# Kernel tuning notes

Hardware: AMD Instinct MI355X
Metric: run time of the kernel (lower is better)

Reference implementation:

```python
import jax, jax.numpy as jnp
import numpy as np

H = 64; W = 64; P = 16; NPH = 4; NPW = 4; PH = 16; PW = 16; ZD = 32; HD = 1024; UD = 3; B = 256


def affine_grid(theta, Ho, Wo):
    # torch F.affine_grid, align_corners=False. theta [N,2,3] -> grid [N,Ho,Wo,2]
    xs = (2.0 * jnp.arange(Wo, dtype=theta.dtype) + 1.0) / Wo - 1.0
    ys = (2.0 * jnp.arange(Ho, dtype=theta.dtype) + 1.0) / Ho - 1.0
    X, Y = jnp.meshgrid(xs, ys)  # [Ho,Wo] each, x varies along last axis
    base = jnp.stack([X, Y, jnp.ones_like(X)], axis=-1)  # [Ho,Wo,3]
    return jnp.einsum('nij,hwj->nhwi', theta, base)


def grid_sample(img, grid):
    # torch F.grid_sample bilinear, padding_mode='zeros', align_corners=False
    # img [N,H,W], grid [N,Ho,Wo,2] in [-1,1]
    Hi, Wi = img.shape[1], img.shape[2]
    x = (grid[..., 0] + 1.0) * Wi / 2.0 - 0.5
    y = (grid[..., 1] + 1.0) * Hi / 2.0 - 0.5
    x0 = jnp.floor(x); y0 = jnp.floor(y)
    wx = x - x0; wy = y - y0

    def gather(ix, iy):
        valid = (ix >= 0) & (ix < Wi) & (iy >= 0) & (iy < Hi)
        ixc = jnp.clip(ix, 0, Wi - 1).astype(jnp.int32)
        iyc = jnp.clip(iy, 0, Hi - 1).astype(jnp.int32)
        v = jax.vmap(lambda im, yy, xx: im[yy, xx])(img, iyc, ixc)
        return jnp.where(valid, v, 0.0)

    return (gather(x0, y0) * (1 - wx) * (1 - wy)
            + gather(x0 + 1, y0) * wx * (1 - wy)
            + gather(x0, y0 + 1) * (1 - wx) * wy
            + gather(x0 + 1, y0 + 1) * wx * wy)


def rot_tr(u):
    # rotTrMatrix: u [N,3] (angle, tx, ty) -> [N,2,3]
    c = jnp.cos(u[:, 0]); s = jnp.sin(u[:, 0])
    R = jnp.stack([jnp.stack([c, -s], -1), jnp.stack([s, c], -1)], -2)  # [N,2,2]
    return jnp.concatenate([R, u[:, 1:3, None]], axis=2)


def anchor_theta():
    # anchor_move: identity rotation + per-part grid-cell-center translations
    tx = (np.arange(NPW) * (W / NPW) + W / NPW / 2) / W - 0.5
    ty = (np.arange(NPH) * (H / NPH) + H / NPH / 2) / H - 0.5
    th = np.tile(np.concatenate([np.eye(2), np.zeros((2, 1))], axis=1)[None], (P, 1, 1)).astype(np.float32)
    for k in range(P):
        th[k, 0, 2] = tx[k % NPW]
        th[k, 1, 2] = ty[k // NPW]
    return jnp.asarray(th)


def forward(inputs, W1, b1, W2, b2, Wum, bum, Wuv, buv, Wgm, bgm, Wgv, bgv, Wz, M, eps_u, eps_g):
    hid = jax.nn.relu(inputs.reshape(-1, H * W) @ W1 + b1)
    hid = jax.nn.relu(hid @ W2 + b2)
    # global transform distribution (note: F.threshold(x,-6,6) -> 6 where x<=-6)
    gmu = jnp.tanh(hid @ Wgm + bgm)
    gpre = hid @ Wgv + bgv
    gvar = jnp.exp(jnp.where(gpre > -6.0, gpre, 6.0))
    gu = gmu + gvar * eps_g  # sample_u uses mu + var*eps (var, not std) as in source
    # per-part transform distribution (F.threshold(x,-6,-6) -> clamp below at -6)
    umu = jnp.tanh(hid @ Wum + bum)
    upre = hid @ Wuv + buv
    uvar = jnp.exp(jnp.where(upre > -6.0, upre, -6.0))
    u = (umu + uvar * eps_u).reshape(-1, UD)  # [B*P,3]
    # decode parts (input is ones, as in source)
    parts = jax.nn.sigmoid(jnp.ones((B, ZD), inputs.dtype) @ Wz).reshape(B * P, PH, PW)
    padh = (H - PH) // 2; padw = (W - PW) // 2
    parts = jnp.pad(parts, ((0, 0), (padh, H - PH - padh), (padw, W - PW - padw)))
    # anchor placement of parts and kernel masks
    th_a = jnp.tile(anchor_theta(), (B, 1, 1))  # [B*P,2,3], part-minor ordering
    g_a = affine_grid(th_a, H, W)
    parts = grid_sample(parts, g_a)                     # [B*P,H,W]
    KM = grid_sample(M[:B * P].reshape(B * P, H, W), g_a)
    # per-part rotation+translation for parts; translation-only for kernel
    theta = rot_tr(u)                                   # [B*P,2,3]
    g = affine_grid(theta, H, W)
    eye = jnp.broadcast_to(jnp.eye(2, dtype=theta.dtype), (B * P, 2, 2))
    theta_K = jnp.concatenate([eye, theta[:, :, 2:3]], axis=2)
    g_K = affine_grid(theta_K, H, W)
    KM = grid_sample(KM, g_K).reshape(B, P, H, W)
    xp = grid_sample(parts, g).reshape(B, P, H, W)
    # masked weighted compositing
    num = jnp.sum(xp * KM, axis=1)
    den = jnp.sum(KM, axis=1)
    den = jnp.where(den == 0.0, 1.0, den)
    x = num / den
    # global transform
    theta_g = rot_tr(gu)
    g_g = affine_grid(theta_g, H, W)
    return grid_sample(x, g_g)[:, None]  # [B,1,H,W]


def setup_inputs() -> dict:
    key = jax.random.key(0)
    ks = jax.random.split(key, 18)

    def lin(k, fin, fout):
        return jax.random.normal(k, (fin, fout), jnp.float32) / np.sqrt(fin)

    return {
        'inputs': jax.random.uniform(ks[0], (B, H * W), jnp.float32),
        'W1': lin(ks[1], H * W, HD), 'b1': jnp.zeros((HD,), jnp.float32),
        'W2': lin(ks[2], HD, HD), 'b2': jnp.zeros((HD,), jnp.float32),
        'Wum': lin(ks[3], HD, P * UD), 'bum': jnp.zeros((P * UD,), jnp.float32),
        'Wuv': lin(ks[4], HD, P * UD), 'buv': jnp.zeros((P * UD,), jnp.float32),
        'Wgm': lin(ks[5], HD, UD), 'bgm': jnp.zeros((UD,), jnp.float32),
        'Wgv': lin(ks[6], HD, UD), 'bgv': jnp.zeros((UD,), jnp.float32),
        'Wz': lin(ks[7], ZD, P * PH * PW),
        'M': jax.random.uniform(ks[8], (B * P, 1, H, W), jnp.float32),
        'eps_u': jax.random.normal(ks[9], (B, P * UD), jnp.float32),
        'eps_g': jax.random.normal(ks[10], (B, UD), jnp.float32),
    }


def reference(inputs, W1, b1, W2, b2, Wum, bum, Wuv, buv, Wgm, bgm, Wgv, bgv, Wz, M, eps_u, eps_g):
    return forward(inputs, W1, b1, W2, b2, Wum, bum, Wuv, buv, Wgm, bgm, Wgv, bgv, Wz, M, eps_u, eps_g)
```

## Files before the change

### kernel.cpp

```cpp
#include <hip/hip_runtime.h>
#include <math.h>

#define SPLITK 8

typedef __bf16 bf16x8 __attribute__((ext_vector_type(8)));
typedef float  f32x4  __attribute__((ext_vector_type(4)));
typedef float  f32x16 __attribute__((ext_vector_type(16)));

__device__ inline unsigned short bf16rne(float x) {
    unsigned int u = __float_as_uint(x);
    unsigned int r = u + 0x7FFFu + ((u >> 16) & 1u);
    return (unsigned short)(r >> 16);
}
__device__ inline float bf16tof(unsigned short h) {
    return __uint_as_float(((unsigned int)h) << 16);
}

__global__ __launch_bounds__(256) void prep_all(
    const float* __restrict__ inputs,
    const float* __restrict__ W1, const float* __restrict__ W2,
    const float* __restrict__ Wum, const float* __restrict__ Wuv,
    const float* __restrict__ Wgm, const float* __restrict__ Wgv,
    const float* __restrict__ Wz,
    unsigned short* __restrict__ Ahi, unsigned short* __restrict__ Alo,
    unsigned short* __restrict__ W1Thi, unsigned short* __restrict__ W1Tlo,
    unsigned short* __restrict__ W2Thi, unsigned short* __restrict__ W2Tlo,
    float* __restrict__ WT, float* __restrict__ partsb)
{
    __shared__ float t[32][33];
    int bid = blockIdx.x;
    int tid = threadIdx.x;
    if (bid < 4096 || (bid >= 5120 && bid < 6144)) {
        const float* W = (bid < 4096) ? W1 : W2;
        unsigned short* Thi = (bid < 4096) ? W1Thi : W2Thi;
        unsigned short* Tlo = (bid < 4096) ? W1Tlo : W2Tlo;
        int K = (bid < 4096) ? 4096 : 1024;
        int b2 = (bid < 4096) ? bid : (bid - 5120);
        int n0 = (b2 & 31) * 32, k0 = (b2 >> 5) * 32;
        int c = tid & 31, r0 = tid >> 5;
#pragma unroll
        for (int i = 0; i < 4; i++)
            t[r0 + 8 * i][c] = W[(size_t)(k0 + r0 + 8 * i) * 1024 + n0 + c];
        __syncthreads();
        int kk = tid & 31, n1 = tid >> 5;
#pragma unroll
        for (int i = 0; i < 4; i++) {
            float x = t[kk][n1 + 8 * i];
            unsigned short h = bf16rne(x);
            unsigned short l = bf16rne(x - bf16tof(h));
            size_t o = (size_t)(n0 + n1 + 8 * i) * K + k0 + kk;
            Thi[o] = h;
            Tlo[o] = l;
        }
    } else if (bid < 5120) {
        int id = ((bid - 4096) * 256 + tid) * 4;
        float4 x = *(const float4*)(inputs + id);
        ushort4 h, l;
        h.x = bf16rne(x.x); l.x = bf16rne(x.x - bf16tof(h.x));
        h.y = bf16rne(x.y); l.y = bf16rne(x.y - bf16tof(h.y));
        h.z = bf16rne(x.z); l.z = bf16rne(x.z - bf16tof(h.z));
        h.w = bf16rne(x.w); l.w = bf16rne(x.w - bf16tof(h.w));
        *(ushort4*)(Ahi + id) = h;
        *(ushort4*)(Alo + id) = l;
    } else if (bid < 6552) {
        int id = (bid - 6144) * 256 + tid;
        int o = id >> 10;
        int k = id & 1023;
        float v;
        if (o < 48)       v = Wum[k * 48 + o];
        else if (o < 96)  v = Wuv[k * 48 + (o - 48)];
        else if (o < 99)  v = Wgm[k * 3 + (o - 96)];
        else              v = Wgv[k * 3 + (o - 99)];
        WT[id] = v;
    } else {
        int idx = (bid - 6552) * 256 + tid;
        float s = 0.f;
#pragma unroll
        for (int z = 0; z < 32; z++) s += Wz[z * 4096 + idx];
        partsb[idx] = 1.f / (1.f + expf(-s));
    }
}

__global__ __launch_bounds__(256) void gemm_bf16x3(
    const unsigned short* __restrict__ Ahi, const unsigned short* __restrict__ Alo,
    const unsigned short* __restrict__ Bhi, const unsigned short* __restrict__ Blo,
    float* __restrict__ psum, int K, int kchunk)
{
    __shared__ unsigned short Ah[4096], Al[4096], Bh[4096], Bl[4096];
    int tid = threadIdx.x;
    int n0 = blockIdx.x * 64, m0 = blockIdx.y * 64;
    int kb = blockIdx.z * kchunk;
    int wid = tid >> 6, lane = tid & 63;
    int wm = wid & 1, wn = wid >> 1;
    int lr = lane & 31, hi = lane >> 5;

    int r0 = tid >> 3, ch0 = tid & 7;
    int r1 = (tid + 256) >> 3, ch1 = (tid + 256) & 7;
    int l0 = r0 * 64 + 8 * (ch0 ^ (r0 & 7));
    int l1 = r1 * 64 + 8 * (ch1 ^ (r1 & 7));
    size_t ga0 = (size_t)(m0 + r0) * K + kb + ch0 * 8;
    size_t ga1 = (size_t)(m0 + r1) * K + kb + ch1 * 8;
    size_t gb0 = (size_t)(n0 + r0) * K + kb + ch0 * 8;
    size_t gb1 = (size_t)(n0 + r1) * K + kb + ch1 * 8;

    f32x16 acc_hh = {}, acc_hl = {}, acc_lh = {};

    int nkt = kchunk >> 6;
    uint4 vah0, vah1, val0, val1, vbh0, vbh1, vbl0, vbl1;
    vah0 = *(const uint4*)(Ahi + ga0);
    vah1 = *(const uint4*)(Ahi + ga1);
    val0 = *(const uint4*)(Alo + ga0);
    val1 = *(const uint4*)(Alo + ga1);
    vbh0 = *(const uint4*)(Bhi + gb0);
    vbh1 = *(const uint4*)(Bhi + gb1);
    vbl0 = *(const uint4*)(Blo + gb0);
    vbl1 = *(const uint4*)(Blo + gb1);

    int basea = (wm * 32 + lr) * 64;
    int baseb = (wn * 32 + lr) * 64;
    int sw = lr & 7;

    for (int kt = 0; kt < nkt; kt++) {
        __syncthreads();
        *(uint4*)(Ah + l0) = vah0;
        *(uint4*)(Ah + l1) = vah1;
        *(uint4*)(Al + l0) = val0;
        *(uint4*)(Al + l1) = val1;
        *(uint4*)(Bh + l0) = vbh0;
        *(uint4*)(Bh + l1) = vbh1;
        *(uint4*)(Bl + l0) = vbl0;
        *(uint4*)(Bl + l1) = vbl1;
        __syncthreads();
        if (kt + 1 < nkt) {
            size_t o = (size_t)(kt + 1) * 64;
            vah0 = *(const uint4*)(Ahi + ga0 + o);
            vah1 = *(const uint4*)(Ahi + ga1 + o);
            val0 = *(const uint4*)(Alo + ga0 + o);
            val1 = *(const uint4*)(Alo + ga1 + o);
            vbh0 = *(const uint4*)(Bhi + gb0 + o);
            vbh1 = *(const uint4*)(Bhi + gb1 + o);
            vbl0 = *(const uint4*)(Blo + gb0 + o);
            vbl1 = *(const uint4*)(Blo + gb1 + o);
        }
#pragma unroll
        for (int s = 0; s < 4; s++) {
            int cidx = 8 * (((s << 1) + hi) ^ sw);
            bf16x8 afh = *(const bf16x8*)(Ah + basea + cidx);
            bf16x8 afl = *(const bf16x8*)(Al + basea + cidx);
            bf16x8 bfh = *(const bf16x8*)(Bh + baseb + cidx);
            bf16x8 bfl = *(const bf16x8*)(Bl + baseb + cidx);
            acc_hh = __builtin_amdgcn_mfma_f32_32x32x16_bf16(afh, bfh, acc_hh, 0, 0, 0);
            acc_hl = __builtin_amdgcn_mfma_f32_32x32x16_bf16(afh, bfl, acc_hl, 0, 0, 0);
            acc_lh = __builtin_amdgcn_mfma_f32_32x32x16_bf16(afl, bfh, acc_lh, 0, 0, 0);
        }
    }

    float* op = psum + (size_t)blockIdx.z * (256 * 1024);
    int colg = n0 + wn * 32 + lr;
#pragma unroll
    for (int r = 0; r < 16; r++) {
        int rowl = (r & 3) + 8 * (r >> 2) + 4 * hi;
        float v = acc_hh[r] + acc_hl[r] + acc_lh[r];
        op[(size_t)(m0 + wm * 32 + rowl) * 1024 + colg] = v;
    }
}

__global__ __launch_bounds__(256) void reduce_bias_relu_split(
    const float* __restrict__ psum, const float* __restrict__ bias,
    unsigned short* __restrict__ hi, unsigned short* __restrict__ lo)
{
    int i = (blockIdx.x * 256 + threadIdx.x) * 4;
    float4 v = *(const float4*)(psum + i);
#pragma unroll
    for (int s = 1; s < SPLITK; s++) {
        float4 t = *(const float4*)(psum + (size_t)s * 262144 + i);
        v.x += t.x; v.y += t.y; v.z += t.z; v.w += t.w;
    }
    float4 bb = *(const float4*)(bias + (i & 1023));
    v.x = fmaxf(v.x + bb.x, 0.f);
    v.y = fmaxf(v.y + bb.y, 0.f);
    v.z = fmaxf(v.z + bb.z, 0.f);
    v.w = fmaxf(v.w + bb.w, 0.f);
    ushort4 h, l;
    h.x = bf16rne(v.x); l.x = bf16rne(v.x - bf16tof(h.x));
    h.y = bf16rne(v.y); l.y = bf16rne(v.y - bf16tof(h.y));
    h.z = bf16rne(v.z); l.z = bf16rne(v.z - bf16tof(h.z));
    h.w = bf16rne(v.w); l.w = bf16rne(v.w - bf16tof(h.w));
    *(ushort4*)(hi + i) = h;
    *(ushort4*)(lo + i) = l;
}

__global__ __launch_bounds__(512) void heads_v3(
    const float* __restrict__ psum, const float* __restrict__ b2,
    const float* __restrict__ WT,
    const float* __restrict__ bum, const float* __restrict__ buv,
    const float* __restrict__ bgm, const float* __restrict__ bgv,
    const float* __restrict__ eps_u, const float* __restrict__ eps_g,
    float* __restrict__ u_out, float* __restrict__ gu_out)
{
    int b = blockIdx.x;
    int tid = threadIdx.x;
    int w = tid >> 6, l = tid & 63;

    float4 hr[4];
#pragma unroll
    for (int i = 0; i < 4; i++) {
        int k = b * 1024 + i * 256 + l * 4;
        float4 acc = *(const float4*)(psum + k);
#pragma unroll
        for (int s = 1; s < SPLITK; s++) {
            float4 t = *(const float4*)(psum + (size_t)s * 262144 + k);
            acc.x += t.x; acc.y += t.y; acc.z += t.z; acc.w += t.w;
        }
        float4 bb = *(const float4*)(b2 + i * 256 + l * 4);
        acc.x = fmaxf(acc.x + bb.x, 0.f);
        acc.y = fmaxf(acc.y + bb.y, 0.f);
        acc.z = fmaxf(acc.z + bb.z, 0.f);
        acc.w = fmaxf(acc.w + bb.w, 0.f);
        hr[i] = acc;
    }

    int o = w;
    int rm = (o < 48) ? o : (48 + o);
    int rv = (o < 48) ? (o + 48) : (51 + o);
    float4 wm[4], wv[4];
    {
        const float* wp = WT + rm * 1024 + l * 4;
#pragma unroll
        for (int i = 0; i < 4; i++) wm[i] = *(const float4*)(wp + i * 256);
        wp = WT + rv * 1024 + l * 4;
#pragma unroll
        for (int i = 0; i < 4; i++) wv[i] = *(const float4*)(wp + i * 256);
    }

    while (o < 51) {
        int onext = o + 8;
        float4 wmn[4], wvn[4];
        if (onext < 51) {
            int rm2 = (onext < 48) ? onext : (48 + onext);
            int rv2 = (onext < 48) ? (onext + 48) : (51 + onext);
            const float* wp = WT + rm2 * 1024 + l * 4;
#pragma unroll
            for (int i = 0; i < 4; i++) wmn[i] = *(const float4*)(wp + i * 256);
            wp = WT + rv2 * 1024 + l * 4;
#pragma unroll
            for (int i = 0; i < 4; i++) wvn[i] = *(const float4*)(wp + i * 256);
        }
        float am = 0.f, av = 0.f;
#pragma unroll
        for (int i = 0; i < 4; i++) {
            am = fmaf(hr[i].x, wm[i].x, am);
            am = fmaf(hr[i].y, wm[i].y, am);
            am = fmaf(hr[i].z, wm[i].z, am);
            am = fmaf(hr[i].w, wm[i].w, am);
            av = fmaf(hr[i].x, wv[i].x, av);
            av = fmaf(hr[i].y, wv[i].y, av);
            av = fmaf(hr[i].z, wv[i].z, av);
            av = fmaf(hr[i].w, wv[i].w, av);
        }
#pragma unroll
        for (int s = 32; s; s >>= 1) {
            am += __shfl_xor(am, s, 64);
            av += __shfl_xor(av, s, 64);
        }
        if (l == 0) {
            if (o < 48) {
                float umu = tanhf(am + bum[o]);
                float uvar = expf(fmaxf(av + buv[o], -6.f));
                u_out[b * 48 + o] = umu + uvar * eps_u[b * 48 + o];
            } else {
                int n = o - 48;
                float gmu = tanhf(am + bgm[n]);
                float gpre = av + bgv[n];
                float gvar = expf(gpre > -6.f ? gpre : 6.f);
                gu_out[b * 3 + n] = gmu + gvar * eps_g[b * 3 + n];
            }
        }
#pragma unroll
        for (int i = 0; i < 4; i++) { wm[i] = wmn[i]; wv[i] = wvn[i]; }
        o = onext;
    }
}

__global__ __launch_bounds__(1024) void composite_final(
    const float* __restrict__ M, const float* __restrict__ parts,
    const float* __restrict__ u, const float* __restrict__ gu,
    float* __restrict__ out)
{
    __shared__ float patch[4096];
    __shared__ float plane[2][4096];
    __shared__ float pc[16], psn[16], ptx[16], pty[16], pwx[16], pwy[16];
    __shared__ int pix[16], piy[16];
    int b = blockIdx.x;
    int tid = threadIdx.x;

    for (int i = tid; i < 4096; i += 1024) patch[i] = parts[i];
    if (tid < 16) {
        const float* up = u + (b * 16 + tid) * 3;
        float ang = up[0];
        pc[tid] = cosf(ang);
        psn[tid] = sinf(ang);
        float tx = up[1], ty = up[2];
        ptx[tid] = tx;
        pty[tid] = ty;
        float ax = fminf(fmaxf(32.f * tx, -16384.f), 16384.f);
        float fax = floorf(ax);
        pwx[tid] = ax - fax;
        pix[tid] = (int)fax;
        float ay = fminf(fmaxf(32.f * ty, -16384.f), 16384.f);
        float fay = floorf(ay);
        pwy[tid] = ay - fay;
        piy[tid] = (int)fay;
    }

    const float* Mb = M + ((size_t)(b * 16) << 12);
    ((float4*)plane[0])[tid] = ((const float4*)Mb)[tid];
    float4 pfn = ((const float4*)(Mb + 4096))[tid];
    __syncthreads();

    int j = tid & 63;
    int i0 = (tid >> 6) * 4;
    float xnv = (float)(2 * j + 1) * (1.f / 64.f) - 1.f;
    float ynv0 = (float)(2 * i0 + 1) * (1.f / 64.f) - 1.f;

    float num[4] = {}, den[4] = {};

    for (int p = 0; p < 16; p++) {
        int cur = p & 1;
        if (p + 1 < 16) ((float4*)plane[1 - cur])[tid] = pfn;
        if (p + 2 < 16) pfn = ((const float4*)(Mb + ((size_t)(p + 2) << 12)))[tid];

        int dx = 8 * (p & 3) - 12;
        int dy = 8 * (p >> 2) - 12;
        float c = pc[p], s = psn[p], tx = ptx[p], ty = pty[p];
        float wx = pwx[p], wy = pwy[p];
        int ix = pix[p], iy = piy[p];
        int iY = iy + dy;

        int x0 = j + ix;
        int X = x0 + dx;
        bool vc0 = ((unsigned)x0 < 64u) && ((unsigned)X < 64u);
        bool vc1 = ((unsigned)(x0 + 1) < 64u) && ((unsigned)(X + 1) < 64u);
        float w0 = vc0 ? (1.f - wx) : 0.f;
        float w1 = vc1 ? wx : 0.f;
        int Xc0 = min(max(X, 0), 63);
        int Xc1 = min(max(X + 1, 0), 63);

        const float* pl = plane[cur];
        float R[5];
#pragma unroll
        for (int r = 0; r < 5; r++) {
            int i = i0 + r;
            int ri = i + iY;
            bool vr = ((unsigned)(i + iy) < 64u) && ((unsigned)ri < 64u);
            int ric = min(max(ri, 0), 63);
            const float* row = pl + (ric << 6);
            float val = fmaf(w0, row[Xc0], w1 * row[Xc1]);
            R[r] = vr ? val : 0.f;
        }

        float gx0 = fmaf(-s, ynv0, fmaf(c, xnv, tx));
        float gy0 = fmaf(c, ynv0, fmaf(s, xnv, ty));
        float xs = fmaf(gx0, 32.f, 31.5f);
        float ysv = fmaf(gy0, 32.f, 31.5f);
        int ox = 24 - dx, oy = 24 - dy;
        float oxf = (float)ox, oyf = (float)oy;
        const float* pp = patch + (p << 8);
#pragma unroll
        for (int r = 0; r < 4; r++) {
            float km = fmaf(wy, R[r + 1] - R[r], R[r]);
            den[r] += km;

            if (xs >= oxf - 1.f && xs < oxf + 16.f &&
                ysv >= oyf - 1.f && ysv < oyf + 16.f) {
                float xf = floorf(xs), yf = floorf(ysv);
                float wxx = xs - xf, wyy = ysv - yf;
                int a0 = (int)yf - oy;
                int b0c = (int)xf - ox;
                float v00 = 0.f, v10 = 0.f, v01 = 0.f, v11 = 0.f;
                if ((unsigned)a0 < 16u) {
                    const float* pr = pp + a0 * 16;
                    if ((unsigned)b0c < 16u) v00 = pr[b0c];
                    if ((unsigned)(b0c + 1) < 16u) v10 = pr[b0c + 1];
                }
                if ((unsigned)(a0 + 1) < 16u) {
                    const float* pr = pp + (a0 + 1) * 16;
                    if ((unsigned)b0c < 16u) v01 = pr[b0c];
                    if ((unsigned)(b0c + 1) < 16u) v11 = pr[b0c + 1];
                }
                float top = fmaf(wxx, v10 - v00, v00);
                float bot = fmaf(wxx, v11 - v01, v01);
                float xp = fmaf(wyy, bot - top, top);
                num[r] = fmaf(xp, km, num[r]);
            }
            xs -= s;
            ysv += c;
        }
        __syncthreads();
    }

    float* xl = plane[0];
#pragma unroll
    for (int r = 0; r < 4; r++) {
        float d = (den[r] == 0.f) ? 1.f : den[r];
        xl[(i0 + r) * 64 + j] = num[r] / d;
    }
    __syncthreads();

    float ang = gu[b * 3 + 0], gtx = gu[b * 3 + 1], gty = gu[b * 3 + 2];
    float cg = cosf(ang), sg = sinf(ang);
    float* ob = out + ((size_t)b << 12);
#pragma unroll
    for (int r = 0; r < 4; r++) {
        int i = i0 + r;
        float ynv = (float)(2 * i + 1) * (1.f / 64.f) - 1.f;
        float gx = cg * xnv - sg * ynv + gtx;
        float gy = sg * xnv + cg * ynv + gty;
        gx = fminf(fmaxf(gx, -8.f), 8.f);
        gy = fminf(fmaxf(gy, -8.f), 8.f);
        float xs = fmaf(gx, 32.f, 31.5f);
        float ysv = fmaf(gy, 32.f, 31.5f);
        float xf = floorf(xs), yf = floorf(ysv);
        float wx = xs - xf, wy = ysv - yf;
        int x0 = (int)xf, y0 = (int)yf;
        float v00 = 0.f, v10 = 0.f, v01 = 0.f, v11 = 0.f;
        bool vx0 = (unsigned)x0 < 64u, vx1 = (unsigned)(x0 + 1) < 64u;
        if ((unsigned)y0 < 64u) {
            const float* row = xl + y0 * 64;
            if (vx0) v00 = row[x0];
            if (vx1) v10 = row[x0 + 1];
        }
        if ((unsigned)(y0 + 1) < 64u) {
            const float* row = xl + (y0 + 1) * 64;
            if (vx0) v01 = row[x0];
            if (vx1) v11 = row[x0 + 1];
        }
        float top = fmaf(wx, v10 - v00, v00);
        float bot = fmaf(wx, v11 - v01, v01);
        ob[i * 64 + j] = fmaf(wy, bot - top, top);
    }
}

extern "C" void kernel_launch(void* const* d_in, const int* in_sizes, int n_in,
                              void* d_out, int out_size, void* d_ws, size_t ws_size,
                              hipStream_t stream)
{
    (void)in_sizes; (void)n_in; (void)out_size; (void)ws_size;
    const float* inputs = (const float*)d_in[0];
    const float* W1  = (const float*)d_in[1];
    const float* b1  = (const float*)d_in[2];
    const float* W2  = (const float*)d_in[3];
    const float* b2  = (const float*)d_in[4];
    const float* Wum = (const float*)d_in[5];
    const float* bum = (const float*)d_in[6];
    const float* Wuv = (const float*)d_in[7];
    const float* buv = (const float*)d_in[8];
    const float* Wgm = (const float*)d_in[9];
    const float* bgm = (const float*)d_in[10];
    const float* Wgv = (const float*)d_in[11];
    const float* bgv = (const float*)d_in[12];
    const float* Wz  = (const float*)d_in[13];
    const float* Mm  = (const float*)d_in[14];
    const float* eps_u = (const float*)d_in[15];
    const float* eps_g = (const float*)d_in[16];

    float* ws = (float*)d_ws;
    float* psum      = ws;
    float* u_buf     = ws + 2097152;
    float* gu_buf    = u_buf + 12288;
    float* parts_buf = gu_buf + 768;
    float* WTh_buf   = parts_buf + 4096;
    unsigned short* us = (unsigned short*)(WTh_buf + 104448);
    unsigned short* Ahi   = us;
    unsigned short* Alo   = Ahi + 1048576;
    unsigned short* W1Thi = Alo + 1048576;
    unsigned short* W1Tlo = W1Thi + 4194304;
    unsigned short* W2Thi = W1Tlo + 4194304;
    unsigned short* W2Tlo = W2Thi + 1048576;
    unsigned short* H1hi  = W2Tlo + 1048576;
    unsigned short* H1lo  = H1hi + 262144;

    prep_all<<<6568, 256, 0, stream>>>(inputs, W1, W2, Wum, Wuv, Wgm, Wgv, Wz,
                                       Ahi, Alo, W1Thi, W1Tlo, W2Thi, W2Tlo,
                                       WTh_buf, parts_buf);

    gemm_bf16x3<<<dim3(16, 4, SPLITK), 256, 0, stream>>>(Ahi, Alo, W1Thi, W1Tlo,
                                                         psum, 4096, 4096 / SPLITK);
    reduce_bias_relu_split<<<256, 256, 0, stream>>>(psum, b1, H1hi, H1lo);
    gemm_bf16x3<<<dim3(16, 4, SPLITK), 256, 0, stream>>>(H1hi, H1lo, W2Thi, W2Tlo,
                                                         psum, 1024, 1024 / SPLITK);
    heads_v3<<<256, 512, 0, stream>>>(psum, b2, WTh_buf, bum, buv, bgm, bgv,
                                      eps_u, eps_g, u_buf, gu_buf);
    composite_final<<<256, 1024, 0, stream>>>(Mm, parts_buf, u_buf, gu_buf,
                                              (float*)d_out);
}
```

Measured before the change: 198.0 us.

## Fuse all stages into one persistent kernel with software grid barriers

Replaces the six separate launches (prep, two split-K GEMMs, reduce, heads, composite) with a single persistent 256-block, 1024-thread kernel that separates phases with an atomic grid barrier. The goal is to remove launch gaps and to keep the head outputs in shared memory instead of going through global buffers. The GEMM tiles drop to a 32-wide K step, and only two of the four thread groups in each block do GEMM work, which halves the active compute during the GEMM phases. It also depends on all 256 blocks being co-resident, or the spin barrier can deadlock.

Measured after the change: 342.8 us. +73.1%, slower.

```diff
diff --git a/kernel.cpp b/kernel.cpp
--- a/kernel.cpp
+++ b/kernel.cpp
@@ -1,306 +1,323 @@
 #include <hip/hip_runtime.h>
 #include <math.h>
 
+#define NBLK 256
 #define SPLITK 8
+#define PSUM_STRIDE 262144
 
 typedef __bf16 bf16x8 __attribute__((ext_vector_type(8)));
-typedef float  f32x4  __attribute__((ext_vector_type(4)));
 typedef float  f32x16 __attribute__((ext_vector_type(16)));
 
-__device__ inline unsigned short bf16rne(float x) {
+__device__ __forceinline__ unsigned short bf16rne(float x) {
     unsigned int u = __float_as_uint(x);
     unsigned int r = u + 0x7FFFu + ((u >> 16) & 1u);
     return (unsigned short)(r >> 16);
 }
-__device__ inline float bf16tof(unsigned short h) {
+__device__ __forceinline__ float bf16tof(unsigned short h) {
     return __uint_as_float(((unsigned int)h) << 16);
 }
 
-__global__ __launch_bounds__(256) void prep_all(
-    const float* __restrict__ inputs,
-    const float* __restrict__ W1, const float* __restrict__ W2,
-    const float* __restrict__ Wum, const float* __restrict__ Wuv,
-    const float* __restrict__ Wgm, const float* __restrict__ Wgv,
-    const float* __restrict__ Wz,
+__device__ __forceinline__ void grid_barrier(unsigned int* bar) {
+    __syncthreads();
+    if (threadIdx.x == 0) {
+        __threadfence();
+        unsigned int gen = __hip_atomic_load(bar + 32, __ATOMIC_RELAXED, __HIP_MEMORY_SCOPE_AGENT);
+        unsigned int arrived = __hip_atomic_fetch_add(bar, 1u, __ATOMIC_ACQ_REL, __HIP_MEMORY_SCOPE_AGENT);
+        if (arrived == (unsigned int)(NBLK - 1)) {
+            __hip_atomic_store(bar, 0u, __ATOMIC_RELAXED, __HIP_MEMORY_SCOPE_AGENT);
+            __hip_atomic_store(bar + 32, gen + 1u, __ATOMIC_RELEASE, __HIP_MEMORY_SCOPE_AGENT);
+        } else {
+            long cap = 0;
+            while (__hip_atomic_load(bar + 32, __ATOMIC_ACQUIRE, __HIP_MEMORY_SCOPE_AGENT) == gen) {
+                __builtin_amdgcn_s_sleep(2);
+                if (++cap > 200000000L) break;
+            }
+        }
+        __threadfence();
+    }
+    __syncthreads();
+}
+
+__device__ __forceinline__ void gemm_job(
+    const unsigned short* __restrict__ Ahi, const unsigned short* __restrict__ Alo,
+    const unsigned short* __restrict__ Bhi, const unsigned short* __restrict__ Blo,
+    float* __restrict__ psum, int K, int kchunk, int job, int t,
+    unsigned short* lds, bool active)
+{
+    unsigned short* Ah = lds;
+    unsigned short* Al = lds + 2048;
+    unsigned short* Bh = lds + 4096;
+    unsigned short* Bl = lds + 6144;
+    int z = job & 7, xy = job >> 3;
+    int n0 = (xy & 15) * 64, m0 = (xy >> 4) * 64;
+    int kb = z * kchunk;
+    int wid = t >> 6, lane = t & 63;
+    int wm = wid & 1, wn = wid >> 1;
+    int lr = lane & 31, hi = lane >> 5;
+
+    int r0 = t >> 2, ch0 = t & 3;
+    int l0 = r0 * 32 + 8 * (ch0 ^ ((r0 >> 1) & 3));
+    size_t ga = (size_t)(m0 + r0) * K + kb + ch0 * 8;
+    size_t gb = (size_t)(n0 + r0) * K + kb + ch0 * 8;
+
+    f32x16 acc_hh = {}, acc_hl = {}, acc_lh = {};
+    int nkt = kchunk >> 5;
+
+    uint4 vah, val, vbh, vbl;
+    if (active) {
+        vah = *(const uint4*)(Ahi + ga);
+        val = *(const uint4*)(Alo + ga);
+        vbh = *(const uint4*)(Bhi + gb);
+        vbl = *(const uint4*)(Blo + gb);
+    }
+
+    int basea = (wm * 32 + lr) * 32;
+    int baseb = (wn * 32 + lr) * 32;
+    int sw = (lr >> 1) & 3;
+
+    for (int kt = 0; kt < nkt; kt++) {
+        __syncthreads();
+        if (active) {
+            *(uint4*)(Ah + l0) = vah;
+            *(uint4*)(Al + l0) = val;
+            *(uint4*)(Bh + l0) = vbh;
+            *(uint4*)(Bl + l0) = vbl;
+        }
+        __syncthreads();
+        if (active) {
+            if (kt + 1 < nkt) {
+                size_t o = (size_t)(kt + 1) * 32;
+                vah = *(const uint4*)(Ahi + ga + o);
+                val = *(const uint4*)(Alo + ga + o);
+                vbh = *(const uint4*)(Bhi + gb + o);
+                vbl = *(const uint4*)(Blo + gb + o);
+            }
+#pragma unroll
+            for (int s = 0; s < 2; s++) {
+                int ca = 8 * (((s << 1) + hi) ^ sw);
+                bf16x8 afh = *(const bf16x8*)(Ah + basea + ca);
+                bf16x8 afl = *(const bf16x8*)(Al + basea + ca);
+                bf16x8 bfh = *(const bf16x8*)(Bh + baseb + ca);
+                bf16x8 bfl = *(const bf16x8*)(Bl + baseb + ca);
+                acc_hh = __builtin_amdgcn_mfma_f32_32x32x16_bf16(afh, bfh, acc_hh, 0, 0, 0);
+                acc_hl = __builtin_amdgcn_mfma_f32_32x32x16_bf16(afh, bfl, acc_hl, 0, 0, 0);
+                acc_lh = __builtin_amdgcn_mfma_f32_32x32x16_bf16(afl, bfh, acc_lh, 0, 0, 0);
+            }
+        }
+    }
+    if (active) {
+        float* op = psum + (size_t)z * PSUM_STRIDE;
+        int colg = n0 + wn * 32 + lr;
+#pragma unroll
+        for (int r = 0; r < 16; r++) {
+            int rowl = (r & 3) + 8 * (r >> 2) + 4 * hi;
+            op[(size_t)(m0 + wm * 32 + rowl) * 1024 + colg] = acc_hh[r] + acc_hl[r] + acc_lh[r];
+        }
+    }
+}
+
+__global__ __launch_bounds__(1024) void mega(
+    const float* __restrict__ inputs, const float* __restrict__ W1,
+    const float* __restrict__ b1, const float* __restrict__ W2,
+    const float* __restrict__ b2,
+    const float* __restrict__ Wum, const float* __restrict__ bum,
+    const float* __restrict__ Wuv, const float* __restrict__ buv,
+    const float* __restrict__ Wgm, const float* __restrict__ bgm,
+    const float* __restrict__ Wgv, const float* __restrict__ bgv,
+    const float* __restrict__ Wz, const float* __restrict__ Mm,
+    const float* __restrict__ eps_u, const float* __restrict__ eps_g,
+    float* __restrict__ out,
+    unsigned int* __restrict__ bar,
+    float* __restrict__ psum, float* __restrict__ parts_buf, float* __restrict__ WT,
     unsigned short* __restrict__ Ahi, unsigned short* __restrict__ Alo,
     unsigned short* __restrict__ W1Thi, unsigned short* __restrict__ W1Tlo,
     unsigned short* __restrict__ W2Thi, unsigned short* __restrict__ W2Tlo,
-    float* __restrict__ WT, float* __restrict__ partsb)
+    unsigned short* __restrict__ H1hi, unsigned short* __restrict__ H1lo)
 {
-    __shared__ float t[32][33];
-    int bid = blockIdx.x;
+    __shared__ __align__(16) unsigned char smem[65536];
+    int blk = blockIdx.x;
+    if (blk >= NBLK) return;
     int tid = threadIdx.x;
-    if (bid < 4096 || (bid >= 5120 && bid < 6144)) {
-        const float* W = (bid < 4096) ? W1 : W2;
-        unsigned short* Thi = (bid < 4096) ? W1Thi : W2Thi;
-        unsigned short* Tlo = (bid < 4096) ? W1Tlo : W2Tlo;
-        int K = (bid < 4096) ? 4096 : 1024;
-        int b2 = (bid < 4096) ? bid : (bid - 5120);
-        int n0 = (b2 & 31) * 32, k0 = (b2 >> 5) * 32;
-        int c = tid & 31, r0 = tid >> 5;
-#pragma unroll
-        for (int i = 0; i < 4; i++)
-            t[r0 + 8 * i][c] = W[(size_t)(k0 + r0 + 8 * i) * 1024 + n0 + c];
-        __syncthreads();
-        int kk = tid & 31, n1 = tid >> 5;
-#pragma unroll
-        for (int i = 0; i < 4; i++) {
-            float x = t[kk][n1 + 8 * i];
-            unsigned short h = bf16rne(x);
-            unsigned short l = bf16rne(x - bf16tof(h));
-            size_t o = (size_t)(n0 + n1 + 8 * i) * K + k0 + kk;
-            Thi[o] = h;
-            Tlo[o] = l;
-        }
-    } else if (bid < 5120) {
-        int id = ((bid - 4096) * 256 + tid) * 4;
-        float4 x = *(const float4*)(inputs + id);
-        ushort4 h, l;
-        h.x = bf16rne(x.x); l.x = bf16rne(x.x - bf16tof(h.x));
-        h.y = bf16rne(x.y); l.y = bf16rne(x.y - bf16tof(h.y));
-        h.z = bf16rne(x.z); l.z = bf16rne(x.z - bf16tof(h.z));
-        h.w = bf16rne(x.w); l.w = bf16rne(x.w - bf16tof(h.w));
-        *(ushort4*)(Ahi + id) = h;
-        *(ushort4*)(Alo + id) = l;
-    } else if (bid < 6552) {
-        int id = (bid - 6144) * 256 + tid;
-        int o = id >> 10;
-        int k = id & 1023;
-        float v;
-        if (o < 48)       v = Wum[k * 48 + o];
-        else if (o < 96)  v = Wuv[k * 48 + (o - 48)];
-        else if (o < 99)  v = Wgm[k * 3 + (o - 96)];
-        else              v = Wgv[k * 3 + (o - 99)];
-        WT[id] = v;
-    } else {
-        int idx = (bid - 6552) * 256 + tid;
-        float s = 0.f;
-#pragma unroll
-        for (int z = 0; z < 32; z++) s += Wz[z * 4096 + idx];
-        partsb[idx] = 1.f / (1.f + expf(-s));
-    }
-}
-
-__global__ __launch_bounds__(256) void gemm_bf16x3(
-    const unsigned short* __restrict__ Ahi, const unsigned short* __restrict__ Alo,
-    const unsigned short* __restrict__ Bhi, const unsigned short* __restrict__ Blo,
-    float* __restrict__ psum, int K, int kchunk)
-{
-    __shared__ unsigned short Ah[4096], Al[4096], Bh[4096], Bl[4096];
-    int tid = threadIdx.x;
-    int n0 = blockIdx.x * 64, m0 = blockIdx.y * 64;
-    int kb = blockIdx.z * kchunk;
-    int wid = tid >> 6, lane = tid & 63;
-    int wm = wid & 1, wn = wid >> 1;
-    int lr = lane & 31, hi = lane >> 5;
-
-    int r0 = tid >> 3, ch0 = tid & 7;
-    int r1 = (tid + 256) >> 3, ch1 = (tid + 256) & 7;
-    int l0 = r0 * 64 + 8 * (ch0 ^ (r0 & 7));
-    int l1 = r1 * 64 + 8 * (ch1 ^ (r1 & 7));
-    size_t ga0 = (size_t)(m0 + r0) * K + kb + ch0 * 8;
-    size_t ga1 = (size_t)(m0 + r1) * K + kb + ch1 * 8;
-    size_t gb0 = (size_t)(n0 + r0) * K + kb + ch0 * 8;
-    size_t gb1 = (size_t)(n0 + r1) * K + kb + ch1 * 8;
-
-    f32x16 acc_hh = {}, acc_hl = {}, acc_lh = {};
-
-    int nkt = kchunk >> 6;
-    uint4 vah0, vah1, val0, val1, vbh0, vbh1, vbl0, vbl1;
-    vah0 = *(const uint4*)(Ahi + ga0);
-    vah1 = *(const uint4*)(Ahi + ga1);
-    val0 = *(const uint4*)(Alo + ga0);
-    val1 = *(const uint4*)(Alo + ga1);
-    vbh0 = *(const uint4*)(Bhi + gb0);
-    vbh1 = *(const uint4*)(Bhi + gb1);
-    vbl0 = *(const uint4*)(Blo + gb0);
-    vbl1 = *(const uint4*)(Blo + gb1);
-
-    int basea = (wm * 32 + lr) * 64;
-    int baseb = (wn * 32 + lr) * 64;
-    int sw = lr & 7;
-
-    for (int kt = 0; kt < nkt; kt++) {
-        __syncthreads();
-        *(uint4*)(Ah + l0) = vah0;
-        *(uint4*)(Ah + l1) = vah1;
-        *(uint4*)(Al + l0) = val0;
-        *(uint4*)(Al + l1) = val1;
-        *(uint4*)(Bh + l0) = vbh0;
-        *(uint4*)(Bh + l1) = vbh1;
-        *(uint4*)(Bl + l0) = vbl0;
-        *(uint4*)(Bl + l1) = vbl1;
-        __syncthreads();
-        if (kt + 1 < nkt) {
-            size_t o = (size_t)(kt + 1) * 64;
-            vah0 = *(const uint4*)(Ahi + ga0 + o);
-            vah1 = *(const uint4*)(Ahi + ga1 + o);
-            val0 = *(const uint4*)(Alo + ga0 + o);
-            val1 = *(const uint4*)(Alo + ga1 + o);
-            vbh0 = *(const uint4*)(Bhi + gb0 + o);
-            vbh1 = *(const uint4*)(Bhi + gb1 + o);
-            vbl0 = *(const uint4*)(Blo + gb0 + o);
-            vbl1 = *(const uint4*)(Blo + gb1 + o);
-        }
-#pragma unroll
-        for (int s = 0; s < 4; s++) {
-            int cidx = 8 * (((s << 1) + hi) ^ sw);
-            bf16x8 afh = *(const bf16x8*)(Ah + basea + cidx);
-            bf16x8 afl = *(const bf16x8*)(Al + basea + cidx);
-            bf16x8 bfh = *(const bf16x8*)(Bh + baseb + cidx);
-            bf16x8 bfl = *(const bf16x8*)(Bl + baseb + cidx);
-            acc_hh = __builtin_amdgcn_mfma_f32_32x32x16_bf16(afh, bfh, acc_hh, 0, 0, 0);
-            acc_hl = __builtin_amdgcn_mfma_f32_32x32x16_bf16(afh, bfl, acc_hl, 0, 0, 0);
-            acc_lh = __builtin_amdgcn_mfma_f32_32x32x16_bf16(afl, bfh, acc_lh, 0, 0, 0);
-        }
-    }
-
-    float* op = psum + (size_t)blockIdx.z * (256 * 1024);
-    int colg = n0 + wn * 32 + lr;
-#pragma unroll
-    for (int r = 0; r < 16; r++) {
-        int rowl = (r & 3) + 8 * (r >> 2) + 4 * hi;
-        float v = acc_hh[r] + acc_hl[r] + acc_lh[r];
-        op[(size_t)(m0 + wm * 32 + rowl) * 1024 + colg] = v;
-    }
-}
-
-__global__ __launch_bounds__(256) void reduce_bias_relu_split(
-    const float* __restrict__ psum, const float* __restrict__ bias,
-    unsigned short* __restrict__ hi, unsigned short* __restrict__ lo)
-{
-    int i = (blockIdx.x * 256 + threadIdx.x) * 4;
-    float4 v = *(const float4*)(psum + i);
-#pragma unroll
-    for (int s = 1; s < SPLITK; s++) {
-        float4 t = *(const float4*)(psum + (size_t)s * 262144 + i);
-        v.x += t.x; v.y += t.y; v.z += t.z; v.w += t.w;
-    }
-    float4 bb = *(const float4*)(bias + (i & 1023));
-    v.x = fmaxf(v.x + bb.x, 0.f);
-    v.y = fmaxf(v.y + bb.y, 0.f);
-    v.z = fmaxf(v.z + bb.z, 0.f);
-    v.w = fmaxf(v.w + bb.w, 0.f);
-    ushort4 h, l;
-    h.x = bf16rne(v.x); l.x = bf16rne(v.x - bf16tof(h.x));
-    h.y = bf16rne(v.y); l.y = bf16rne(v.y - bf16tof(h.y));
-    h.z = bf16rne(v.z); l.z = bf16rne(v.z - bf16tof(h.z));
-    h.w = bf16rne(v.w); l.w = bf16rne(v.w - bf16tof(h.w));
-    *(ushort4*)(hi + i) = h;
-    *(ushort4*)(lo + i) = l;
-}
-
-__global__ __launch_bounds__(512) void heads_v3(
-    const float* __restrict__ psum, const float* __restrict__ b2,
-    const float* __restrict__ WT,
-    const float* __restrict__ bum, const float* __restrict__ buv,
-    const float* __restrict__ bgm, const float* __restrict__ bgv,
-    const float* __restrict__ eps_u, const float* __restrict__ eps_g,
-    float* __restrict__ u_out, float* __restrict__ gu_out)
-{
-    int b = blockIdx.x;
-    int tid = threadIdx.x;
-    int w = tid >> 6, l = tid & 63;
-
-    float4 hr[4];
-#pragma unroll
-    for (int i = 0; i < 4; i++) {
-        int k = b * 1024 + i * 256 + l * 4;
-        float4 acc = *(const float4*)(psum + k);
-#pragma unroll
-        for (int s = 1; s < SPLITK; s++) {
-            float4 t = *(const float4*)(psum + (size_t)s * 262144 + k);
-            acc.x += t.x; acc.y += t.y; acc.z += t.z; acc.w += t.w;
-        }
-        float4 bb = *(const float4*)(b2 + i * 256 + l * 4);
-        acc.x = fmaxf(acc.x + bb.x, 0.f);
-        acc.y = fmaxf(acc.y + bb.y, 0.f);
-        acc.z = fmaxf(acc.z + bb.z, 0.f);
-        acc.w = fmaxf(acc.w + bb.w, 0.f);
-        hr[i] = acc;
-    }
-
-    int o = w;
-    int rm = (o < 48) ? o : (48 + o);
-    int rv = (o < 48) ? (o + 48) : (51 + o);
-    float4 wm[4], wv[4];
+    int g = tid >> 8;
+    int t = tid & 255;
+    int gid = blk * 1024 + tid;
+
     {
-        const float* wp = WT + rm * 1024 + l * 4;
-#pragma unroll
-        for (int i = 0; i < 4; i++) wm[i] = *(const float4*)(wp + i * 256);
-        wp = WT + rv * 1024 + l * 4;
-#pragma unroll
-        for (int i = 0; i < 4; i++) wv[i] = *(const float4*)(wp + i * 256);
-    }
-
-    while (o < 51) {
-        int onext = o + 8;
-        float4 wmn[4], wvn[4];
-        if (onext < 51) {
-            int rm2 = (onext < 48) ? onext : (48 + onext);
-            int rv2 = (onext < 48) ? (onext + 48) : (51 + onext);
-            const float* wp = WT + rm2 * 1024 + l * 4;
-#pragma unroll
-            for (int i = 0; i < 4; i++) wmn[i] = *(const float4*)(wp + i * 256);
-            wp = WT + rv2 * 1024 + l * 4;
-#pragma unroll
-            for (int i = 0; i < 4; i++) wvn[i] = *(const float4*)(wp + i * 256);
-        }
-        float am = 0.f, av = 0.f;
-#pragma unroll
-        for (int i = 0; i < 4; i++) {
-            am = fmaf(hr[i].x, wm[i].x, am);
-            am = fmaf(hr[i].y, wm[i].y, am);
-            am = fmaf(hr[i].z, wm[i].z, am);
-            am = fmaf(hr[i].w, wm[i].w, am);
-            av = fmaf(hr[i].x, wv[i].x, av);
-            av = fmaf(hr[i].y, wv[i].y, av);
-            av = fmaf(hr[i].z, wv[i].z, av);
-            av = fmaf(hr[i].w, wv[i].w, av);
-        }
-#pragma unroll
-        for (int s = 32; s; s >>= 1) {
-            am += __shfl_xor(am, s, 64);
-            av += __shfl_xor(av, s, 64);
-        }
-        if (l == 0) {
-            if (o < 48) {
-                float umu = tanhf(am + bum[o]);
-                float uvar = expf(fmaxf(av + buv[o], -6.f));
-                u_out[b * 48 + o] = umu + uvar * eps_u[b * 48 + o];
-            } else {
-                int n = o - 48;
-                float gmu = tanhf(am + bgm[n]);
-                float gpre = av + bgv[n];
-                float gvar = expf(gpre > -6.f ? gpre : 6.f);
-                gu_out[b * 3 + n] = gmu + gvar * eps_g[b * 3 + n];
-            }
-        }
-#pragma unroll
-        for (int i = 0; i < 4; i++) { wm[i] = wmn[i]; wv[i] = wvn[i]; }
-        o = onext;
-    }
-}
-
-__global__ __launch_bounds__(1024) void composite_final(
-    const float* __restrict__ M, const float* __restrict__ parts,
-    const float* __restrict__ u, const float* __restrict__ gu,
-    float* __restrict__ out)
-{
-    __shared__ float patch[4096];
-    __shared__ float plane[2][4096];
-    __shared__ float pc[16], psn[16], ptx[16], pty[16], pwx[16], pwy[16];
-    __shared__ int pix[16], piy[16];
-    int b = blockIdx.x;
-    int tid = threadIdx.x;
-
-    for (int i = tid; i < 4096; i += 1024) patch[i] = parts[i];
+        float (*tile)[33] = (float(*)[33])(smem + g * 4352);
+        for (int pass = 0; pass < 4; pass++) {
+            int b2t = blk * 16 + pass * 4 + g;
+            int n0 = (b2t & 31) * 32, k0 = (b2t >> 5) * 32;
+            int c = t & 31, r0 = t >> 5;
+#pragma unroll
+            for (int i = 0; i < 4; i++)
+                tile[r0 + 8 * i][c] = W1[(size_t)(k0 + r0 + 8 * i) * 1024 + n0 + c];
+            __syncthreads();
+            int kk = t & 31, n1 = t >> 5;
+#pragma unroll
+            for (int i = 0; i < 4; i++) {
+                float x = tile[kk][n1 + 8 * i];
+                unsigned short h = bf16rne(x);
+                unsigned short l = bf16rne(x - bf16tof(h));
+                size_t o = (size_t)(n0 + n1 + 8 * i) * 4096 + k0 + kk;
+                W1Thi[o] = h;
+                W1Tlo[o] = l;
+            }
+            __syncthreads();
+        }
+        {
+            int b2t = blk * 4 + g;
+            int n0 = (b2t & 31) * 32, k0 = (b2t >> 5) * 32;
+            int c = t & 31, r0 = t >> 5;
+#pragma unroll
+            for (int i = 0; i < 4; i++)
+                tile[r0 + 8 * i][c] = W2[(size_t)(k0 + r0 + 8 * i) * 1024 + n0 + c];
+            __syncthreads();
+            int kk = t & 31, n1 = t >> 5;
+#pragma unroll
+            for (int i = 0; i < 4; i++) {
+                float x = tile[kk][n1 + 8 * i];
+                unsigned short h = bf16rne(x);
+                unsigned short l = bf16rne(x - bf16tof(h));
+                size_t o = (size_t)(n0 + n1 + 8 * i) * 1024 + k0 + kk;
+                W2Thi[o] = h;
+                W2Tlo[o] = l;
+            }
+        }
+        {
+            int id = gid * 4;
+            float4 x = *(const float4*)(inputs + id);
+            ushort4 h, l;
+            h.x = bf16rne(x.x); l.x = bf16rne(x.x - bf16tof(h.x));
+            h.y = bf16rne(x.y); l.y = bf16rne(x.y - bf16tof(h.y));
+            h.z = bf16rne(x.z); l.z = bf16rne(x.z - bf16tof(h.z));
+            h.w = bf16rne(x.w); l.w = bf16rne(x.w - bf16tof(h.w));
+            *(ushort4*)(Ahi + id) = h;
+            *(ushort4*)(Alo + id) = l;
+        }
+        if (gid < 104448) {
+            int o = gid >> 10;
+            int k = gid & 1023;
+            float v;
+            if (o < 48)       v = Wum[k * 48 + o];
+            else if (o < 96)  v = Wuv[k * 48 + (o - 48)];
+            else if (o < 99)  v = Wgm[k * 3 + (o - 96)];
+            else              v = Wgv[k * 3 + (o - 99)];
+            WT[gid] = v;
+        }
+        if (gid < 4096) {
+            float s = 0.f;
+#pragma unroll
+            for (int z = 0; z < 32; z++) s += Wz[z * 4096 + gid];
+            parts_buf[gid] = 1.f / (1.f + expf(-s));
+        }
+    }
+    grid_barrier(bar);
+
+    gemm_job(Ahi, Alo, W1Thi, W1Tlo, psum, 4096, 4096 / SPLITK,
+             blk * 2 + (g & 1), t, (unsigned short*)(smem + g * 16384), g < 2);
+    grid_barrier(bar);
+
+    {
+        float v = psum[gid];
+#pragma unroll
+        for (int s = 1; s < SPLITK; s++) v += psum[(size_t)s * PSUM_STRIDE + gid];
+        v = fmaxf(v + b1[tid], 0.f);
+        unsigned short h = bf16rne(v);
+        unsigned short l = bf16rne(v - bf16tof(h));
+        H1hi[gid] = h;
+        H1lo[gid] = l;
+    }
+    grid_barrier(bar);
+
+    gemm_job(H1hi, H1lo, W2Thi, W2Tlo, psum, 1024, 1024 / SPLITK,
+             blk * 2 + (g & 1), t, (unsigned short*)(smem + g * 16384), g < 2);
+    grid_barrier(bar);
+
+    float* patch  = (float*)smem;
+    float* plane0 = (float*)(smem + 16384);
+    float* plane1 = (float*)(smem + 32768);
+    float* h2     = (float*)(smem + 49152);
+    float* u_raw  = (float*)(smem + 53248);
+    float* pc  = (float*)(smem + 53504);
+    float* psn = pc + 16;
+    float* ptx = pc + 32;
+    float* pty = pc + 48;
+    float* pwx = pc + 64;
+    float* pwy = pc + 80;
+    int*   pix = (int*)(pc + 96);
+    int*   piy = pix + 16;
+    int b = blk;
+
+    {
+        float v = psum[(size_t)b * 1024 + tid];
+#pragma unroll
+        for (int s = 1; s < SPLITK; s++)
+            v += psum[(size_t)s * PSUM_STRIDE + (size_t)b * 1024 + tid];
+        h2[tid] = fmaxf(v + b2[tid], 0.f);
+    }
+    for (int i = tid; i < 4096; i += 1024) patch[i] = parts_buf[i];
+    __syncthreads();
+    {
+        int w = tid >> 6, l = tid & 63;
+        const float4* h4 = (const float4*)h2;
+        float4 hr0 = h4[l], hr1 = h4[64 + l], hr2 = h4[128 + l], hr3 = h4[192 + l];
+        for (int o = w; o < 51; o += 16) {
+            int rm = (o < 48) ? o : (48 + o);
+            int rv = (o < 48) ? (o + 48) : (51 + o);
+            const float* wpm = WT + rm * 1024 + l * 4;
+            const float* wpv = WT + rv * 1024 + l * 4;
+            float4 wm0 = *(const float4*)(wpm);
+            float4 wm1 = *(const float4*)(wpm + 256);
+            float4 wm2 = *(const float4*)(wpm + 512);
+            float4 wm3 = *(const float4*)(wpm + 768);
+            float4 wv0 = *(const float4*)(wpv);
+            float4 wv1 = *(const float4*)(wpv + 256);
+            float4 wv2 = *(const float4*)(wpv + 512);
+            float4 wv3 = *(const float4*)(wpv + 768);
+            float am = 0.f, av = 0.f;
+            am = fmaf(hr0.x, wm0.x, am); am = fmaf(hr0.y, wm0.y, am);
+            am = fmaf(hr0.z, wm0.z, am); am = fmaf(hr0.w, wm0.w, am);
+            av = fmaf(hr0.x, wv0.x, av); av = fmaf(hr0.y, wv0.y, av);
+            av = fmaf(hr0.z, wv0.z, av); av = fmaf(hr0.w, wv0.w, av);
+            am = fmaf(hr1.x, wm1.x, am); am = fmaf(hr1.y, wm1.y, am);
+            am = fmaf(hr1.z, wm1.z, am); am = fmaf(hr1.w, wm1.w, am);
+            av = fmaf(hr1.x, wv1.x, av); av = fmaf(hr1.y, wv1.y, av);
+            av = fmaf(hr1.z, wv1.z, av); av = fmaf(hr1.w, wv1.w, av);
+            am = fmaf(hr2.x, wm2.x, am); am = fmaf(hr2.y, wm2.y, am);
+            am = fmaf(hr2.z, wm2.z, am); am = fmaf(hr2.w, wm2.w, am);
+            av = fmaf(hr2.x, wv2.x, av); av = fmaf(hr2.y, wv2.y, av);
+            av = fmaf(hr2.z, wv2.z, av); av = fmaf(hr2.w, wv2.w, av);
+            am = fmaf(hr3.x, wm3.x, am); am = fmaf(hr3.y, wm3.y, am);
+            am = fmaf(hr3.z, wm3.z, am); am = fmaf(hr3.w, wm3.w, am);
+            av = fmaf(hr3.x, wv3.x, av); av = fmaf(hr3.y, wv3.y, av);
+            av = fmaf(hr3.z, wv3.z, av); av = fmaf(hr3.w, wv3.w, av);
+#pragma unroll
+            for (int s = 32; s; s >>= 1) {
+                am += __shfl_xor(am, s, 64);
+                av += __shfl_xor(av, s, 64);
+            }
+            if (l == 0) {
+                if (o < 48) {
+                    float umu = tanhf(am + bum[o]);
+                    float uvar = expf(fmaxf(av + buv[o], -6.f));
+                    u_raw[o] = umu + uvar * eps_u[b * 48 + o];
+                } else {
+                    int n = o - 48;
+                    float gmu = tanhf(am + bgm[n]);
+                    float gpre = av + bgv[n];
+                    float gvar = expf(gpre > -6.f ? gpre : 6.f);
+                    u_raw[o] = gmu + gvar * eps_g[b * 3 + n];
+                }
+            }
+        }
+    }
+    __syncthreads();
+
     if (tid < 16) {
-        const float* up = u + (b * 16 + tid) * 3;
-        float ang = up[0];
+        float ang = u_raw[tid * 3 + 0];
+        float tx = u_raw[tid * 3 + 1], ty = u_raw[tid * 3 + 2];
         pc[tid] = cosf(ang);
         psn[tid] = sinf(ang);
-        float tx = up[1], ty = up[2];
         ptx[tid] = tx;
         pty[tid] = ty;
         float ax = fminf(fmaxf(32.f * tx, -16384.f), 16384.f);
@@ -312,9 +329,8 @@
         pwy[tid] = ay - fay;
         piy[tid] = (int)fay;
     }
-
-    const float* Mb = M + ((size_t)(b * 16) << 12);
-    ((float4*)plane[0])[tid] = ((const float4*)Mb)[tid];
+    const float* Mb = Mm + ((size_t)(b * 16) << 12);
+    ((float4*)plane0)[tid] = ((const float4*)Mb)[tid];
     float4 pfn = ((const float4*)(Mb + 4096))[tid];
     __syncthreads();
 
@@ -324,10 +340,11 @@
     float ynv0 = (float)(2 * i0 + 1) * (1.f / 64.f) - 1.f;
 
     float num[4] = {}, den[4] = {};
+    float* pl_cur = plane0;
+    float* pl_nxt = plane1;
 
     for (int p = 0; p < 16; p++) {
-        int cur = p & 1;
-        if (p + 1 < 16) ((float4*)plane[1 - cur])[tid] = pfn;
+        if (p + 1 < 16) ((float4*)pl_nxt)[tid] = pfn;
         if (p + 2 < 16) pfn = ((const float4*)(Mb + ((size_t)(p + 2) << 12)))[tid];
 
         int dx = 8 * (p & 3) - 12;
@@ -346,7 +363,7 @@
         int Xc0 = min(max(X, 0), 63);
         int Xc1 = min(max(X + 1, 0), 63);
 
-        const float* pl = plane[cur];
+        const float* pl = pl_cur;
         float R[5];
 #pragma unroll
         for (int r = 0; r < 5; r++) {
@@ -397,9 +414,10 @@
             ysv += c;
         }
         __syncthreads();
-    }
-
-    float* xl = plane[0];
+        float* tmp = pl_cur; pl_cur = pl_nxt; pl_nxt = tmp;
+    }
+
+    float* xl = plane0;
 #pragma unroll
     for (int r = 0; r < 4; r++) {
         float d = (den[r] == 0.f) ? 1.f : den[r];
@@ -407,7 +425,7 @@
     }
     __syncthreads();
 
-    float ang = gu[b * 3 + 0], gtx = gu[b * 3 + 1], gty = gu[b * 3 + 2];
+    float ang = u_raw[48], gtx = u_raw[49], gty = u_raw[50];
     float cg = cosf(ang), sg = sinf(ang);
     float* ob = out + ((size_t)b << 12);
 #pragma unroll
@@ -464,13 +482,12 @@
     const float* eps_u = (const float*)d_in[15];
     const float* eps_g = (const float*)d_in[16];
 
+    unsigned int* bar = (unsigned int*)d_ws;
     float* ws = (float*)d_ws;
-    float* psum      = ws;
-    float* u_buf     = ws + 2097152;
-    float* gu_buf    = u_buf + 12288;
-    float* parts_buf = gu_buf + 768;
-    float* WTh_buf   = parts_buf + 4096;
-    unsigned short* us = (unsigned short*)(WTh_buf + 104448);
+    float* psum      = ws + 64;
+    float* parts_buf = psum + 8 * 262144;
+    float* WT_buf    = parts_buf + 4096;
+    unsigned short* us = (unsigned short*)(WT_buf + 104448);
     unsigned short* Ahi   = us;
     unsigned short* Alo   = Ahi + 1048576;
     unsigned short* W1Thi = Alo + 1048576;
@@ -480,17 +497,10 @@
     unsigned short* H1hi  = W2Tlo + 1048576;
     unsigned short* H1lo  = H1hi + 262144;
 
-    prep_all<<<6568, 256, 0, stream>>>(inputs, W1, W2, Wum, Wuv, Wgm, Wgv, Wz,
-                                       Ahi, Alo, W1Thi, W1Tlo, W2Thi, W2Tlo,
-                                       WTh_buf, parts_buf);
-
-    gemm_bf16x3<<<dim3(16, 4, SPLITK), 256, 0, stream>>>(Ahi, Alo, W1Thi, W1Tlo,
-                                                         psum, 4096, 4096 / SPLITK);
-    reduce_bias_relu_split<<<256, 256, 0, stream>>>(psum, b1, H1hi, H1lo);
-    gemm_bf16x3<<<dim3(16, 4, SPLITK), 256, 0, stream>>>(H1hi, H1lo, W2Thi, W2Tlo,
-                                                         psum, 1024, 1024 / SPLITK);
-    heads_v3<<<256, 512, 0, stream>>>(psum, b2, WTh_buf, bum, buv, bgm, bgv,
-                                      eps_u, eps_g, u_buf, gu_buf);
-    composite_final<<<256, 1024, 0, stream>>>(Mm, parts_buf, u_buf, gu_buf,
-                                              (float*)d_out);
+    hipMemsetAsync(d_ws, 0, 256, stream);
+    mega<<<dim3(NBLK), dim3(1024), 0, stream>>>(
+        inputs, W1, b1, W2, b2, Wum, bum, Wuv, buv, Wgm, bgm, Wgv, bgv,
+        Wz, Mm, eps_u, eps_g, (float*)d_out,
+        bar, psum, parts_buf, WT_buf,
+        Ahi, Alo, W1Thi, W1Tlo, W2Thi, W2Tlo, H1hi, H1lo);
 }
```
